# Kernel tuning notes

Hardware: AMD Instinct MI355X
Metric: run time of the kernel (lower is better)

The kernel has to match this reference:

```python
import jax, jax.numpy as jnp
import numpy as np

B, M, C_IN, H, W = 8, 64, 2048, 16, 16
IMG = 512          # image size in pixels (feature stride 32)
OUT = 7            # ROIAlign output size
SCALE = 1.0 / 32.0
SR = 2             # samples per bin; equals ceil(roi_extent/7) for the generated boxes (sampling_ratio=0 behavior)
C2 = C_IN // 2     # 1024
D_ROI, D_BOX = 1024, 256
D_PAIR = 2 * (D_ROI + D_BOX)   # 2560
D_G = D_PAIR // 2              # 1280


def setup_inputs() -> dict:
    key = jax.random.key(0)
    ks = jax.random.split(key, 12)
    s = 0.02
    im_feat = jax.random.normal(ks[0], (B, C_IN, H, W), jnp.float32)
    # XYXY boxes; sizes in (230,440)px so scaled roi extent is in (7,14] -> adaptive sampling ratio == 2
    xy1 = jax.random.uniform(ks[1], (B, M, 2), jnp.float32, 0.0, 60.0)
    wh = jax.random.uniform(ks[2], (B, M, 2), jnp.float32, 230.0, 440.0)
    boxes = jnp.concatenate([xy1, xy1 + wh], -1)
    normalized_boxes = boxes / IMG
    params = dict(
        proj_w=jax.random.normal(ks[3], (C2, C_IN), jnp.float32) * s, proj_b=jnp.zeros((C2,), jnp.float32),
        conv_w=jax.random.normal(ks[4], (256, C2, 3, 3), jnp.float32) * s, conv_b=jnp.zeros((256,), jnp.float32),
        bn_g=jnp.ones((256,), jnp.float32), bn_b=jnp.zeros((256,), jnp.float32),
        bn_m=jnp.zeros((256,), jnp.float32), bn_v=jnp.ones((256,), jnp.float32),
        fc_w=jax.random.normal(ks[5], (D_ROI, 256 * OUT * OUT), jnp.float32) * s, fc_b=jnp.zeros((D_ROI,), jnp.float32),
        ln1_g=jnp.ones((D_ROI,), jnp.float32), ln1_b=jnp.zeros((D_ROI,), jnp.float32),
        box_w=jax.random.normal(ks[6], (D_BOX, 4), jnp.float32) * s, box_b=jnp.zeros((D_BOX,), jnp.float32),
        ln2_g=jnp.ones((D_BOX,), jnp.float32), ln2_b=jnp.zeros((D_BOX,), jnp.float32),
        g1_w=jax.random.normal(ks[7], (D_G, D_PAIR), jnp.float32) * s, g1_b=jnp.zeros((D_G,), jnp.float32),
        g2_w=jax.random.normal(ks[8], (D_G, D_G), jnp.float32) * s, g2_b=jnp.zeros((D_G,), jnp.float32),
        g3_w=jax.random.normal(ks[9], (D_G, D_G), jnp.float32) * s, g3_b=jnp.zeros((D_G,), jnp.float32),
    )
    return dict(im_feat=im_feat, boxes=boxes, normalized_boxes=normalized_boxes, **params)


def _layer_norm(x, g, b, eps=1e-5):
    mu = x.mean(-1, keepdims=True)
    var = ((x - mu) ** 2).mean(-1, keepdims=True)
    return (x - mu) * jax.lax.rsqrt(var + eps) * g + b


def _roi_align(feat, rois, bidx):
    # feat [B,C,Hf,Wf]; rois [N,4] XYXY image coords; bidx [N] int. ROIAlignV2 (aligned=True), 2x2 samples/bin.
    Hf, Wf = feat.shape[2], feat.shape[3]
    x1 = rois[:, 0] * SCALE - 0.5
    y1 = rois[:, 1] * SCALE - 0.5
    bw = (rois[:, 2] - rois[:, 0]) * SCALE / OUT
    bh = (rois[:, 3] - rois[:, 1]) * SCALE / OUT
    ii = (jnp.arange(OUT * SR, dtype=jnp.float32) + 0.5) / SR  # sample offsets in bin units
    xs = x1[:, None] + bw[:, None] * ii[None, :]               # [N, OUT*SR]
    ys = y1[:, None] + bh[:, None] * ii[None, :]

    def interp1(v, size):
        valid = (v >= -1.0) & (v <= size)
        v = jnp.clip(v, 0.0, None)
        lo = jnp.floor(v).astype(jnp.int32)
        over = lo >= size - 1
        lo = jnp.where(over, size - 1, lo)
        v = jnp.where(over, lo.astype(v.dtype), v)
        hi = jnp.where(over, lo, lo + 1)
        return lo, hi, v - lo, valid

    def bilin(b, ys_, xs_):
        img = feat[b]  # [C,Hf,Wf]
        yl, yh, wy, vy = interp1(ys_, Hf)
        xl, xh, wx, vx = interp1(xs_, Wf)
        g = lambda yi, xi: img[:, yi][:, :, xi]  # [C,S,S]
        val = (g(yl, xl) * (1 - wy)[None, :, None] * (1 - wx)[None, None, :]
               + g(yl, xh) * (1 - wy)[None, :, None] * wx[None, None, :]
               + g(yh, xl) * wy[None, :, None] * (1 - wx)[None, None, :]
               + g(yh, xh) * wy[None, :, None] * wx[None, None, :])
        mask = (vy[:, None] & vx[None, :]).astype(val.dtype)
        return val * mask

    vals = jax.vmap(bilin)(bidx, ys, xs)  # [N,C,OUT*SR,OUT*SR]
    N, C = vals.shape[0], vals.shape[1]
    return vals.reshape(N, C, OUT, SR, OUT, SR).mean((3, 5))  # avg over samples per bin


def reference(im_feat, boxes, normalized_boxes, proj_w, proj_b, conv_w, conv_b, bn_g, bn_b, bn_m, bn_v,
              fc_w, fc_b, ln1_g, ln1_b, box_w, box_b, ln2_g, ln2_b, g1_w, g1_b, g2_w, g2_b, g3_w, g3_b):
    # 1x1 conv projection
    x = jnp.einsum('bchw,oc->bohw', im_feat, proj_w) + proj_b[None, :, None, None]
    rois = boxes.reshape(B * M, 4)
    bidx = jnp.repeat(jnp.arange(B), M)
    r = _roi_align(x, rois, bidx)  # [BM, C2, 7, 7]
    # roi_processor: conv3x3 -> BN(eval) -> ReLU -> flatten -> Linear -> ReLU
    r = jax.lax.conv_general_dilated(r, conv_w, (1, 1), 'SAME',
                                     dimension_numbers=('NCHW', 'OIHW', 'NCHW')) + conv_b[None, :, None, None]
    r = (r - bn_m[None, :, None, None]) * jax.lax.rsqrt(bn_v + 1e-5)[None, :, None, None] \
        * bn_g[None, :, None, None] + bn_b[None, :, None, None]
    r = jax.nn.relu(r)
    r = jax.nn.relu(r.reshape(B * M, -1) @ fc_w.T + fc_b)
    r = _layer_norm(r, ln1_g, ln1_b)                       # [BM, 1024]
    nb = normalized_boxes.reshape(B * M, 4) * 2.0 - 1.0
    bf = _layer_norm(nb @ box_w.T + box_b, ln2_g, ln2_b)   # [BM, 256]
    feats = jnp.concatenate([r, bf], -1).reshape(B, M, D_ROI + D_BOX)

    def rel(xm):  # relation network over one image's M rois
        xi = jnp.broadcast_to(xm[None, :, :], (M, M, D_ROI + D_BOX))  # xi[a,b]=x[b]
        xj = jnp.broadcast_to(xm[:, None, :], (M, M, D_ROI + D_BOX))  # xj[a,b]=x[a]
        p = jnp.concatenate([xi, xj], -1).reshape(M * M, D_PAIR)
        h = jax.nn.relu(p @ g1_w.T + g1_b)
        h = jax.nn.relu(h @ g2_w.T + g2_b)
        h = jax.nn.relu(h @ g3_w.T + g3_b)
        return h.sum(0)

    return jax.vmap(rel)(feats)  # [B, 1280]
```

## Files before the change

kernel.cpp:

```cpp
#include <hip/hip_runtime.h>
#include <hip/hip_bf16.h>

typedef __attribute__((ext_vector_type(8))) short short8;
typedef __attribute__((ext_vector_type(4))) float floatx4;
typedef unsigned short u16;

#define GLDS16(gp, lp) __builtin_amdgcn_global_load_lds(                        \
    (const __attribute__((address_space(1))) void*)(gp),                        \
    (__attribute__((address_space(3))) void*)(lp), 16, 0, 0)

__device__ inline u16 f2bf(float f) {
    unsigned u = __float_as_uint(f);
    unsigned r = (u + 0x7fffu + ((u >> 16) & 1u)) >> 16;
    return (u16)r;
}

__device__ inline void block_reduce2(float& s, float& ss) {
    #pragma unroll
    for (int o = 32; o > 0; o >>= 1) {
        s  += __shfl_down(s, o);
        ss += __shfl_down(ss, o);
    }
    __shared__ float red[8];
    const int t = threadIdx.x;
    if ((t & 63) == 0) { red[t >> 6] = s; red[4 + (t >> 6)] = ss; }
    __syncthreads();
    s  = red[0] + red[1] + red[2] + red[3];
    ss = red[4] + red[5] + red[6] + red[7];
}

template<int AMODE, int EPI, int CMODE>
__global__ __launch_bounds__(256)
void gemm_bf16(const u16* __restrict__ A, const u16* __restrict__ B,
               const float* __restrict__ P1, const float* __restrict__ P2,
               void* __restrict__ Cv,
               int M, int N, int Kc, int lda, int ldb, int ldc)
{
    __shared__ short As[2][4096];
    __shared__ short Bs[2][4096];

    const int t  = threadIdx.x;
    const int w  = t >> 6, l = t & 63;
    const int wr = w >> 1, wc = w & 1;
    const int l16 = l & 15, lr = l >> 4;

    const int nwg = gridDim.x * gridDim.y;
    const int bid = blockIdx.y * gridDim.x + blockIdx.x;
    const int cpx = nwg >> 3;
    const int sw  = (bid & 7) * cpx + (bid >> 3);
    const int n0 = (sw % gridDim.x) * 128;
    const int m0 = (sw / gridDim.x) * 128;
    const int kbase = blockIdx.z * Kc;

    const int srow  = w * 16 + (l >> 2);
    const int skoff = (l & 3) * 8;

    const u16* aRow0 = nullptr; const u16* aRow1 = nullptr;
    size_t aSp0 = 0, aSp1 = 0;
    if (AMODE == 0) {
        aRow0 = A + (size_t)(m0 + srow) * lda + kbase + skoff;
        aRow1 = A + (size_t)(m0 + 64 + srow) * lda + kbase + skoff;
    } else {
        const int r0 = m0 + srow, r1 = r0 + 64;
        const int roi0 = r0 / 49, sp0 = r0 - roi0 * 49;
        const int roi1 = r1 / 49, sp1 = r1 - roi1 * 49;
        aSp0 = ((size_t)roi0 * 81 + (sp0 / 7) * 9 + (sp0 % 7)) * 1024 + skoff;
        aSp1 = ((size_t)roi1 * 81 + (sp1 / 7) * 9 + (sp1 % 7)) * 1024 + skoff;
    }
    const u16* bRow0 = B + (size_t)(n0 + srow) * ldb + kbase + skoff;
    const u16* bRow1 = B + (size_t)(n0 + 64 + srow) * ldb + kbase + skoff;

    auto stage = [&](int buf, int k0) {
        if (AMODE == 0) {
            GLDS16(aRow0 + k0, As[buf] + w * 512);
            GLDS16(aRow1 + k0, As[buf] + 2048 + w * 512);
        } else {
            const int kk  = kbase + k0;
            const int tap = kk >> 10;
            const size_t off = (size_t)((tap / 3) * 9 + (tap % 3)) * 1024 + (kk & 1023);
            GLDS16(A + aSp0 + off, As[buf] + w * 512);
            GLDS16(A + aSp1 + off, As[buf] + 2048 + w * 512);
        }
        GLDS16(bRow0 + k0, Bs[buf] + w * 512);
        GLDS16(bRow1 + k0, Bs[buf] + 2048 + w * 512);
    };

    floatx4 acc[4][4] = {};

    stage(0, 0);
    asm volatile("s_waitcnt vmcnt(0)" ::: "memory");
    __builtin_amdgcn_s_barrier();
    __builtin_amdgcn_sched_barrier(0);

    int cur = 0;
    for (int k0 = 0; k0 < Kc; k0 += 32) {
        const int nxt = k0 + 32;
        if (nxt < Kc) stage(cur ^ 1, nxt);

        const short* as = As[cur];
        const short* bs = Bs[cur];
        short8 af[4], bfr[4];
        #pragma unroll
        for (int i = 0; i < 4; ++i)
            af[i] = *reinterpret_cast<const short8*>(&as[(wr * 64 + i * 16 + l16) * 32 + lr * 8]);
        #pragma unroll
        for (int j = 0; j < 4; ++j)
            bfr[j] = *reinterpret_cast<const short8*>(&bs[(wc * 64 + j * 16 + l16) * 32 + lr * 8]);
        #pragma unroll
        for (int i = 0; i < 4; ++i)
            #pragma unroll
            for (int j = 0; j < 4; ++j)
                acc[i][j] = __builtin_amdgcn_mfma_f32_16x16x32_bf16(af[i], bfr[j], acc[i][j], 0, 0, 0);

        asm volatile("s_waitcnt vmcnt(0)" ::: "memory");
        __builtin_amdgcn_s_barrier();
        __builtin_amdgcn_sched_barrier(0);
        cur ^= 1;
    }

    const int mBase = m0 + wr * 64;
    const int nBase = n0 + wc * 64;

    if (CMODE == 2) {
        __shared__ float red2[2][128];
        float csum[4];
        #pragma unroll
        for (int j = 0; j < 4; ++j) {
            const int n = nBase + j * 16 + l16;
            const float b1 = P1[n];
            float s = 0.f;
            #pragma unroll
            for (int i = 0; i < 4; ++i)
                #pragma unroll
                for (int r = 0; r < 4; ++r)
                    s += fmaxf(acc[i][j][r] + b1, 0.f);
            s += __shfl_xor(s, 16);
            s += __shfl_xor(s, 32);
            csum[j] = s;
        }
        __syncthreads();
        if (l < 16) {
            #pragma unroll
            for (int j = 0; j < 4; ++j)
                red2[wr][wc * 64 + j * 16 + l16] = csum[j];
        }
        __syncthreads();
        float* C = (float*)Cv + (size_t)(m0 >> 12) * ldc;
        if (t < 128) atomicAdd(&C[n0 + t], red2[0][t] + red2[1][t]);
        return;
    }

    #pragma unroll
    for (int i = 0; i < 4; ++i) {
        #pragma unroll
        for (int j = 0; j < 4; ++j) {
            const int n = nBase + j * 16 + l16;
            const float b1 = (EPI >= 1) ? P1[n] : 0.f;
            const float b2 = (EPI == 3) ? P2[n] : 0.f;
            #pragma unroll
            for (int r = 0; r < 4; ++r) {
                float v = acc[i][j][r];
                if (EPI == 1)      v += b1;
                else if (EPI == 2) v = fmaxf(v + b1, 0.f);
                else if (EPI == 3) v = fmaxf(v * b1 + b2, 0.f);
                const int m = mBase + i * 16 + lr * 4 + r;
                if (CMODE == 0)      ((float*)Cv)[(size_t)m * ldc + n] = v;
                else if (CMODE == 4) ((u16*)Cv)[(size_t)m * ldc + n] = f2bf(v);
                else if (CMODE == 3) atomicAdd(&((float*)Cv)[(size_t)m * ldc + n], v);
                else if (CMODE == 1) {
                    const int roi = m / 49, sp = m - roi * 49;
                    ((u16*)Cv)[(size_t)roi * 12544 + n * 49 + sp] = f2bf(v);
                }
            }
        }
    }
}

__global__ __launch_bounds__(256)
void transpose_proj(const float* __restrict__ in, u16* __restrict__ out)
{
    __shared__ float tile[64][65];
    const int b = blockIdx.z;
    const int c0 = blockIdx.y * 64;
    const int h0 = blockIdx.x * 64;
    const int t = threadIdx.x;
    const float* src = in + ((size_t)b * 2048 + c0) * 256 + h0;
    #pragma unroll
    for (int p = 0; p < 16; ++p) {
        const int idx = p * 256 + t;
        const int r = idx >> 6, c = idx & 63;
        tile[r][c] = src[(size_t)r * 256 + c];
    }
    __syncthreads();
    u16* dst = out + ((size_t)b * 256 + h0) * 2048 + c0;
    #pragma unroll
    for (int p = 0; p < 16; ++p) {
        const int idx = p * 256 + t;
        const int r = idx >> 6, c = idx & 63;
        dst[(size_t)r * 2048 + c] = f2bf(tile[c][r]);
    }
}

__global__ __launch_bounds__(256)
void zero_halo(u16* __restrict__ r_pad)
{
    const int blk = blockIdx.x;
    const int roi = blk >> 5, h = blk & 31;
    int p;
    if (h < 9)       p = h;
    else if (h < 18) p = 72 + (h - 9);
    else { const int r = (h - 18) >> 1, s = (h - 18) & 1; p = (r + 1) * 9 + s * 8; }
    uint2* o = reinterpret_cast<uint2*>(r_pad + ((size_t)roi * 81 + p) * 1024);
    o[threadIdx.x] = make_uint2(0u, 0u);
}

__global__ __launch_bounds__(256)
void roialign_kernel(const float* __restrict__ x_cl, const float* __restrict__ boxes,
                     u16* __restrict__ r_pad)
{
    const int blk = blockIdx.x;
    const int n = blk / 49, bin = blk % 49;
    const int py = bin / 7, px = bin % 7;
    const int b = n >> 6;
    const float* roi = boxes + n * 4;
    const float x1 = roi[0] * (1.f/32.f) - 0.5f;
    const float y1 = roi[1] * (1.f/32.f) - 0.5f;
    const float bw = (roi[2] - roi[0]) * (1.f/32.f) * (1.0f / 7.0f);
    const float bh = (roi[3] - roi[1]) * (1.f/32.f) * (1.0f / 7.0f);
    const int t = threadIdx.x;

    float acc[4] = {0.f, 0.f, 0.f, 0.f};
    #pragma unroll
    for (int sy = 0; sy < 2; ++sy) {
        #pragma unroll
        for (int sx = 0; sx < 2; ++sx) {
            const float yv = y1 + bh * ((float)(py * 2 + sy) + 0.5f) * 0.5f;
            const float xv = x1 + bw * ((float)(px * 2 + sx) + 0.5f) * 0.5f;
            const bool vy = (yv >= -1.0f) && (yv <= 16.0f);
            const bool vx = (xv >= -1.0f) && (xv <= 16.0f);
            if (!(vy && vx)) continue;
            float yc = fmaxf(yv, 0.f);
            int yl = (int)floorf(yc);
            int yh; if (yl >= 15) { yl = 15; yc = 15.f; yh = 15; } else yh = yl + 1;
            const float wy = yc - (float)yl;
            float xc = fmaxf(xv, 0.f);
            int xl = (int)floorf(xc);
            int xh; if (xl >= 15) { xl = 15; xc = 15.f; xh = 15; } else xh = xl + 1;
            const float wx = xc - (float)xl;

            const float w00 = (1.f - wy) * (1.f - wx), w01 = (1.f - wy) * wx;
            const float w10 = wy * (1.f - wx),         w11 = wy * wx;
            const float* p00 = x_cl + ((size_t)b * 256 + yl * 16 + xl) * 1024;
            const float* p01 = x_cl + ((size_t)b * 256 + yl * 16 + xh) * 1024;
            const float* p10 = x_cl + ((size_t)b * 256 + yh * 16 + xl) * 1024;
            const float* p11 = x_cl + ((size_t)b * 256 + yh * 16 + xh) * 1024;
            #pragma unroll
            for (int cc = 0; cc < 4; ++cc) {
                const int c = t + cc * 256;
                acc[cc] += w00 * p00[c] + w01 * p01[c] + w10 * p10[c] + w11 * p11[c];
            }
        }
    }
    u16* o = r_pad + ((size_t)n * 81 + (py + 1) * 9 + (px + 1)) * 1024;
    #pragma unroll
    for (int cc = 0; cc < 4; ++cc) o[t + cc * 256] = f2bf(acc[cc] * 0.25f);
}

__global__ __launch_bounds__(256)
void pack_conv(const float* __restrict__ conv_w, const float* __restrict__ conv_b,
               const float* __restrict__ bn_g, const float* __restrict__ bn_b,
               const float* __restrict__ bn_m, const float* __restrict__ bn_v,
               u16* __restrict__ wpack, float* __restrict__ scale, float* __restrict__ shift)
{
    const long idx = (long)blockIdx.x * 256 + threadIdx.x;
    if (idx < 2359296L) {
        const int oc = (int)(idx / 9216), k = (int)(idx % 9216);
        const int tap = k >> 10, ic = k & 1023;
        wpack[idx] = f2bf(conv_w[(long)oc * 9216 + ic * 9 + tap]);
    }
    if (idx < 256) {
        const float s = bn_g[idx] * rsqrtf(bn_v[idx] + 1e-5f);
        scale[idx] = s;
        shift[idx] = (conv_b[idx] - bn_m[idx]) * s + bn_b[idx];
    }
}

__global__ __launch_bounds__(256)
void cvt_bf16(const float* __restrict__ in, u16* __restrict__ out, int n4)
{
    const int i = blockIdx.x * 256 + threadIdx.x;
    if (i < n4) {
        const float4 v = reinterpret_cast<const float4*>(in)[i];
        ushort4 o; o.x = f2bf(v.x); o.y = f2bf(v.y); o.z = f2bf(v.z); o.w = f2bf(v.w);
        reinterpret_cast<ushort4*>(out)[i] = o;
    }
}

__global__ __launch_bounds__(256)
void pack_g1(const float* __restrict__ g1w, u16* __restrict__ out)
{
    const int j = blockIdx.x * 256 + threadIdx.x;
    if (j >= 2560 * 320) return;
    const int np = j / 320, k4 = (j - np * 320) * 4;
    const int srow = (np < 1280) ? np : np - 1280;
    const int soff = (np < 1280) ? 0 : 1280;
    const float4 v = *reinterpret_cast<const float4*>(&g1w[(size_t)srow * 2560 + soff + k4]);
    ushort4 o; o.x = f2bf(v.x); o.y = f2bf(v.y); o.z = f2bf(v.z); o.w = f2bf(v.w);
    *reinterpret_cast<ushort4*>(&out[(size_t)np * 1280 + k4]) = o;
}

__global__ __launch_bounds__(256)
void ln1_kernel(const float* __restrict__ in, const float* __restrict__ fb,
                const float* __restrict__ g, const float* __restrict__ b,
                u16* __restrict__ feats)
{
    const int n = blockIdx.x, t = threadIdx.x;
    float4 v = *reinterpret_cast<const float4*>(in + (size_t)n * 1024 + t * 4);
    const float4 bb = *reinterpret_cast<const float4*>(fb + t * 4);
    v.x = fmaxf(v.x + bb.x, 0.f); v.y = fmaxf(v.y + bb.y, 0.f);
    v.z = fmaxf(v.z + bb.z, 0.f); v.w = fmaxf(v.w + bb.w, 0.f);
    float s  = v.x + v.y + v.z + v.w;
    float ss = v.x*v.x + v.y*v.y + v.z*v.z + v.w*v.w;
    block_reduce2(s, ss);
    const float mu  = s * (1.f / 1024.f);
    const float var = ss * (1.f / 1024.f) - mu * mu;
    const float r   = rsqrtf(var + 1e-5f);
    const float4 gp = *reinterpret_cast<const float4*>(g + t * 4);
    const float4 bp = *reinterpret_cast<const float4*>(b + t * 4);
    ushort4 o;
    o.x = f2bf((v.x - mu) * r * gp.x + bp.x);
    o.y = f2bf((v.y - mu) * r * gp.y + bp.y);
    o.z = f2bf((v.z - mu) * r * gp.z + bp.z);
    o.w = f2bf((v.w - mu) * r * gp.w + bp.w);
    *reinterpret_cast<ushort4*>(feats + (size_t)n * 1280 + t * 4) = o;
}

__global__ __launch_bounds__(256)
void box_kernel(const float* __restrict__ nb, const float* __restrict__ bw,
                const float* __restrict__ bb, const float* __restrict__ g,
                const float* __restrict__ be, u16* __restrict__ feats)
{
    const int n = blockIdx.x, j = threadIdx.x;
    const float4 q = *reinterpret_cast<const float4*>(nb + n * 4);
    const float4 w = *reinterpret_cast<const float4*>(bw + j * 4);
    const float v = (q.x * 2.f - 1.f) * w.x + (q.y * 2.f - 1.f) * w.y
                  + (q.z * 2.f - 1.f) * w.z + (q.w * 2.f - 1.f) * w.w + bb[j];
    float s = v, ss = v * v;
    block_reduce2(s, ss);
    const float mu  = s * (1.f / 256.f);
    const float var = ss * (1.f / 256.f) - mu * mu;
    feats[(size_t)n * 1280 + 1024 + j] = f2bf((v - mu) * rsqrtf(var + 1e-5f) * g[j] + be[j]);
}

__global__ __launch_bounds__(256)
void pair_kernel(const float* __restrict__ UV, const float* __restrict__ g1b,
                 u16* __restrict__ h1, int imgbase)
{
    const int pidx = blockIdx.y;
    const int img = imgbase + (pidx >> 12);
    const int a = (pidx >> 6) & 63, b = pidx & 63;
    const int col = blockIdx.x * 256 + threadIdx.x;
    const float v = UV[(size_t)(img * 64 + b) * 2560 + col]
                  + UV[(size_t)(img * 64 + a) * 2560 + 1280 + col] + g1b[col];
    h1[(size_t)pidx * 1280 + col] = f2bf(fmaxf(v, 0.f));
}

__global__ void zero_f32(float* __restrict__ p, int n) {
    const int i = blockIdx.x * 256 + threadIdx.x;
    if (i < n) p[i] = 0.f;
}

extern "C" void kernel_launch(void* const* d_in, const int* in_sizes, int n_in,
                              void* d_out, int out_size, void* d_ws, size_t ws_size,
                              hipStream_t stream)
{
    const float* im_feat = (const float*)d_in[0];
    const float* boxes   = (const float*)d_in[1];
    const float* nboxes  = (const float*)d_in[2];
    const float* proj_w  = (const float*)d_in[3];
    const float* proj_b  = (const float*)d_in[4];
    const float* conv_w  = (const float*)d_in[5];
    const float* conv_b  = (const float*)d_in[6];
    const float* bn_g    = (const float*)d_in[7];
    const float* bn_b    = (const float*)d_in[8];
    const float* bn_m    = (const float*)d_in[9];
    const float* bn_v    = (const float*)d_in[10];
    const float* fc_w    = (const float*)d_in[11];
    const float* fc_b    = (const float*)d_in[12];
    const float* ln1_g   = (const float*)d_in[13];
    const float* ln1_b   = (const float*)d_in[14];
    const float* box_w   = (const float*)d_in[15];
    const float* box_b   = (const float*)d_in[16];
    const float* ln2_g   = (const float*)d_in[17];
    const float* ln2_b   = (const float*)d_in[18];
    const float* g1_w    = (const float*)d_in[19];
    const float* g1_b    = (const float*)d_in[20];
    const float* g2_w    = (const float*)d_in[21];
    const float* g2_b    = (const float*)d_in[22];
    const float* g3_w    = (const float*)d_in[23];
    const float* g3_b    = (const float*)d_in[24];
    float* out = (float*)d_out;
    (void)in_sizes; (void)n_in; (void)out_size; (void)ws_size;

    char* base = (char*)d_ws;
    size_t o = 0;
    auto carve = [&](size_t bytes) { char* p = base + o; o += (bytes + 15) & ~(size_t)15; return p; };
    float* x_cl    = (float*)carve(8388608);
    u16*   imT     = (u16*)  carve(8388608);
    u16*   convout = (u16*)  carve(12845056);
    float* fc_out  = (float*)carve(2097152);
    u16*   feats   = (u16*)  carve(1310720);
    float* UV      = (float*)carve(5242880);
    u16*   wpack   = (u16*)  carve(4718592);
    float* scale   = (float*)carve(1024);
    float* shift   = (float*)carve(1024);
    u16*   projwb  = (u16*)  carve(4194304);
    u16*   fcwb    = (u16*)  carve(25690112);
    u16*   g1wb    = (u16*)  carve(6553600);
    u16*   g2wb    = (u16*)  carve(3276800);
    u16*   g3wb    = (u16*)  carve(3276800);
    char*  big     = carve(84934656);
    u16*   r_pad   = (u16*)big;
    u16*   h1      = (u16*)big;
    u16*   h2      = (u16*)(big + 41943040);

    zero_f32<<<40, 256, 0, stream>>>(out, 10240);
    zero_f32<<<2048, 256, 0, stream>>>(fc_out, 524288);
    zero_f32<<<5120, 256, 0, stream>>>(UV, 1310720);

    cvt_bf16<<<2048, 256, 0, stream>>>(proj_w, projwb, 524288);
    cvt_bf16<<<12544, 256, 0, stream>>>(fc_w, fcwb, 3211264);
    cvt_bf16<<<1600, 256, 0, stream>>>(g2_w, g2wb, 409600);
    cvt_bf16<<<1600, 256, 0, stream>>>(g3_w, g3wb, 409600);
    pack_g1<<<3200, 256, 0, stream>>>(g1_w, g1wb);
    pack_conv<<<9216, 256, 0, stream>>>(conv_w, conv_b, bn_g, bn_b, bn_m, bn_v, wpack, scale, shift);

    transpose_proj<<<dim3(4, 32, 8), 256, 0, stream>>>(im_feat, imT);
    gemm_bf16<0, 1, 0><<<dim3(8, 16, 1), 256, 0, stream>>>(
        imT, projwb, proj_b, nullptr, x_cl, 2048, 1024, 2048, 2048, 2048, 1024);

    zero_halo<<<16384, 256, 0, stream>>>(r_pad);
    roialign_kernel<<<25088, 256, 0, stream>>>(x_cl, boxes, r_pad);

    gemm_bf16<2, 3, 1><<<dim3(2, 196, 1), 256, 0, stream>>>(
        r_pad, wpack, scale, shift, convout, 25088, 256, 9216, 0, 9216, 0);

    gemm_bf16<0, 0, 3><<<dim3(8, 4, 4), 256, 0, stream>>>(
        convout, fcwb, nullptr, nullptr, fc_out, 512, 1024, 3136, 12544, 12544, 1024);

    ln1_kernel<<<512, 256, 0, stream>>>(fc_out, fc_b, ln1_g, ln1_b, feats);
    box_kernel<<<512, 256, 0, stream>>>(nboxes, box_w, box_b, ln2_g, ln2_b, feats);

    gemm_bf16<0, 0, 3><<<dim3(20, 4, 2), 256, 0, stream>>>(
        feats, g1wb, nullptr, nullptr, UV, 512, 2560, 640, 1280, 1280, 2560);

    for (int h = 0; h < 2; ++h) {
        pair_kernel<<<dim3(5, 16384), 256, 0, stream>>>(UV, g1_b, h1, h * 4);
        gemm_bf16<0, 2, 4><<<dim3(10, 128, 1), 256, 0, stream>>>(
            h1, g2wb, g2_b, nullptr, h2, 16384, 1280, 1280, 1280, 1280, 1280);
        gemm_bf16<0, 2, 2><<<dim3(10, 128, 1), 256, 0, stream>>>(
            h2, g3wb, g3_b, nullptr, out + h * 4 * 1280, 16384, 1280, 1280, 1280, 1280, 1280);
    }
}
```

Measured before the change: 939.8 us.

## Triple-buffer GEMM LDS pipeline with XOR-swizzled layout and MFMA priority

Moves the bf16 GEMM from a double-buffered to a triple-buffered global_load_lds pipeline, keeping two K-steps of loads in flight with partial vmcnt waits. It also XOR-swizzles the 16-byte k-chunks in LDS to reduce bank conflicts on fragment reads, and raises wave priority around the MFMA block. The cost is 50% more LDS per block, which can lower occupancy, plus an extra barrier per step. The loop also assumes at least three K-steps per split.

```diff
diff --git a/kernel.cpp b/kernel.cpp
--- a/kernel.cpp
+++ b/kernel.cpp
@@ -36,8 +36,8 @@
                void* __restrict__ Cv,
                int M, int N, int Kc, int lda, int ldb, int ldc)
 {
-    __shared__ short As[2][4096];
-    __shared__ short Bs[2][4096];
+    __shared__ short As[3][4096];
+    __shared__ short Bs[3][4096];
 
     const int t  = threadIdx.x;
     const int w  = t >> 6, l = t & 63;
@@ -53,7 +53,7 @@
     const int kbase = blockIdx.z * Kc;
 
     const int srow  = w * 16 + (l >> 2);
-    const int skoff = (l & 3) * 8;
+    const int skoff = (((l & 3) ^ ((l >> 2) & 3)) * 8);
 
     const u16* aRow0 = nullptr; const u16* aRow1 = nullptr;
     size_t aSp0 = 0, aSp1 = 0;
@@ -87,35 +87,56 @@
 
     floatx4 acc[4][4] = {};
 
-    stage(0, 0);
-    asm volatile("s_waitcnt vmcnt(0)" ::: "memory");
-    __builtin_amdgcn_s_barrier();
-    __builtin_amdgcn_sched_barrier(0);
-
-    int cur = 0;
-    for (int k0 = 0; k0 < Kc; k0 += 32) {
-        const int nxt = k0 + 32;
-        if (nxt < Kc) stage(cur ^ 1, nxt);
-
-        const short* as = As[cur];
-        const short* bs = Bs[cur];
+    auto compute = [&](int buf) {
+        const short* as = As[buf];
+        const short* bs = Bs[buf];
         short8 af[4], bfr[4];
         #pragma unroll
-        for (int i = 0; i < 4; ++i)
-            af[i] = *reinterpret_cast<const short8*>(&as[(wr * 64 + i * 16 + l16) * 32 + lr * 8]);
-        #pragma unroll
-        for (int j = 0; j < 4; ++j)
-            bfr[j] = *reinterpret_cast<const short8*>(&bs[(wc * 64 + j * 16 + l16) * 32 + lr * 8]);
+        for (int i = 0; i < 4; ++i) {
+            const int row = wr * 64 + i * 16 + l16;
+            af[i] = *reinterpret_cast<const short8*>(&as[row * 32 + ((lr ^ (row & 3)) * 8)]);
+        }
+        #pragma unroll
+        for (int j = 0; j < 4; ++j) {
+            const int row = wc * 64 + j * 16 + l16;
+            bfr[j] = *reinterpret_cast<const short8*>(&bs[row * 32 + ((lr ^ (row & 3)) * 8)]);
+        }
+        __builtin_amdgcn_s_setprio(1);
         #pragma unroll
         for (int i = 0; i < 4; ++i)
             #pragma unroll
             for (int j = 0; j < 4; ++j)
                 acc[i][j] = __builtin_amdgcn_mfma_f32_16x16x32_bf16(af[i], bfr[j], acc[i][j], 0, 0, 0);
-
+        __builtin_amdgcn_s_setprio(0);
+    };
+
+    const int nsteps = Kc >> 5;
+
+    stage(0, 0); stage(1, 32); stage(2, 64);
+
+    for (int i = 0; i < nsteps - 2; ++i) {
+        asm volatile("s_waitcnt vmcnt(8)" ::: "memory");
+        __builtin_amdgcn_s_barrier();
+        __builtin_amdgcn_sched_barrier(0);
+        compute(i % 3);
+        __builtin_amdgcn_sched_barrier(0);
+        __builtin_amdgcn_s_barrier();
+        __builtin_amdgcn_sched_barrier(0);
+        if (i < nsteps - 3) stage(i % 3, (i + 3) * 32);
+    }
+    {
+        const int i = nsteps - 2;
+        asm volatile("s_waitcnt vmcnt(4)" ::: "memory");
+        __builtin_amdgcn_s_barrier();
+        __builtin_amdgcn_sched_barrier(0);
+        compute(i % 3);
+    }
+    {
+        const int i = nsteps - 1;
         asm volatile("s_waitcnt vmcnt(0)" ::: "memory");
         __builtin_amdgcn_s_barrier();
         __builtin_amdgcn_sched_barrier(0);
-        cur ^= 1;
+        compute(i % 3);
     }
 
     const int mBase = m0 + wr * 64;
```

Result: no change. 937.2 us (-0.3%).
